# Optimization experiments

Hardware: AMD Instinct MI355X
Metric: run time of the kernel (lower is better)

## Reference

```python
import jax, jax.numpy as jnp
import numpy as np

B, NH, M, XD = 8192, 128, 4096, 1024
ALPHA_1, SIGMA_1 = 100.0, 0.02
MAX_ITER = 30  # FastBarrierProjectionNoUpper(max_iter=30)


def cayley(W):
    """Cayley orthogonalization of a (possibly rectangular) matrix (out, in)."""
    cout, cin = W.shape
    if cout < cin:
        return cayley(W.T).T
    U, V = W[:cin], W[cin:]                 # U: (cin,cin), V: (cout-cin,cin)
    I = jnp.eye(cin, dtype=W.dtype)
    A = U - U.T + V.T @ V                   # skew + Gram
    iIpA = jnp.linalg.inv(I + A)
    return jnp.concatenate([iIpA @ (I - A), -2.0 * V @ iIpA], axis=0)


def cayley_linear(x, W, b, alpha):
    Q = cayley(alpha * W / jnp.linalg.norm(W))
    return x @ Q.T + b


def project_no_upper(lower, f_tilde):
    """Projection of f_tilde onto {f : sum(f)=0, f >= lower} per row.
    f*(lam) = max(f_tilde - lam, lower); Newton on g(lam)=sum f*(lam)=0,
    iterated a fixed MAX_ITER times (matches the 30-iter barrier solver)."""
    lam0 = jnp.mean(f_tilde, axis=-1, keepdims=True)

    def step(lam, _):
        f = jnp.maximum(f_tilde - lam, lower)
        g = jnp.sum(f, axis=-1, keepdims=True)
        active = jnp.sum((f_tilde - lam > lower).astype(f.dtype), axis=-1, keepdims=True)
        dg = -jnp.maximum(active, 1.0)      # g'(lam), safeguarded
        return lam - g / dg, None

    lam, _ = jax.lax.scan(step, lam0, None, length=MAX_ITER)
    return jnp.maximum(f_tilde - lam, lower)


def setup_inputs() -> dict:
    key = jax.random.key(0)
    ks = jax.random.split(key, 8)
    h = jax.random.uniform(ks[0], (B, NH), dtype=jnp.float32)
    h = h / jnp.sum(h, axis=-1, keepdims=True)      # state lives on the simplex
    x = jax.random.normal(ks[1], (B, XD), dtype=jnp.float32)

    def mk_w(k, shape):
        return jax.random.normal(k, shape, dtype=jnp.float32) * 0.05

    W_hm = mk_w(ks[2], (M, NH))
    W_mm = mk_w(ks[3], (M, M))
    W_mh = mk_w(ks[4], (NH, M))
    W_ux = mk_w(ks[5], (M, XD))
    b_hm = jnp.zeros((M,), jnp.float32)
    b_mm = jnp.zeros((M,), jnp.float32)
    b_mh = jnp.zeros((NH,), jnp.float32)
    b_ux = jnp.zeros((M,), jnp.float32)
    # CayleyLinear alpha initialized to ||W||_F (so alpha*W/||W|| == W at init)
    a_hm = jnp.linalg.norm(W_hm)
    a_mm = jnp.linalg.norm(W_mm)
    a_mh = jnp.linalg.norm(W_mh)
    a_ux = jnp.linalg.norm(W_ux)
    return {"h": h, "x": x,
            "W_hm": W_hm, "b_hm": b_hm, "a_hm": a_hm,
            "W_mm": W_mm, "b_mm": b_mm, "a_mm": a_mm,
            "W_mh": W_mh, "b_mh": b_mh, "a_mh": a_mh,
            "W_ux": W_ux, "b_ux": b_ux, "a_ux": a_ux}


def reference(h, x, W_hm, b_hm, a_hm, W_mm, b_mm, a_mm,
              W_mh, b_mh, a_mh, W_ux, b_ux, a_ux):
    # _h_dot_raw (dropout identity in eval mode)
    z = cayley_linear(h, W_hm, b_hm, a_hm) + cayley_linear(x, W_ux, b_ux, a_ux)
    z = jax.nn.relu(z)
    z = jax.nn.relu(cayley_linear(z, W_mm, b_mm, a_mm))
    f_tilde = cayley_linear(z, W_mh, b_mh, a_mh)   # [B, NH]
    # barrier lower bound keeping h >= 0 forward-invariant
    lower = -ALPHA_1 * (jnp.exp(SIGMA_1 * h) - 1.0)
    return project_no_upper(lower, f_tilde)
```

## Files before the change

kernel.cpp:

```cpp
#include <hip/hip_runtime.h>
#include <math.h>

#define ALPHA_1 100.0f
#define SIGMA_1 0.02f

typedef unsigned short bf16_t;
typedef short  bf16x8  __attribute__((ext_vector_type(8)));
typedef float  floatx4 __attribute__((ext_vector_type(4)));

typedef __attribute__((address_space(1))) void glb_void;
typedef __attribute__((address_space(3))) void lds_void;

__device__ __forceinline__ float bf2f(bf16_t u){ return __uint_as_float(((unsigned)u)<<16); }
__device__ __forceinline__ bf16_t f2bf(float f){
  unsigned u = __float_as_uint(f);
  u += 0x7FFFu + ((u>>16)&1u);
  return (bf16_t)(u>>16);
}

__device__ __forceinline__ void split4(float4 v, ushort4& h, ushort4& l){
  h.x=f2bf(v.x); h.y=f2bf(v.y); h.z=f2bf(v.z); h.w=f2bf(v.w);
  l.x=f2bf(v.x-bf2f(h.x)); l.y=f2bf(v.y-bf2f(h.y));
  l.z=f2bf(v.z-bf2f(h.z)); l.w=f2bf(v.w-bf2f(h.w));
}

__device__ __forceinline__ float4 load4f(const float* p){ return *(const float4*)p; }
__device__ __forceinline__ float loadS(const float* p){ return *p; }
__device__ __forceinline__ float loadS(const bf16_t* p){ return bf2f(*p); }
__device__ __forceinline__ void storeS(float* p, float v){ *p = v; }
__device__ __forceinline__ void storeS(bf16_t* p, float v){ *p = f2bf(v); }

__device__ __forceinline__ void async_copy16(void* lds, const void* g){
  __builtin_amdgcn_global_load_lds((glb_void*)g, (lds_void*)lds, 16, 0, 0);
}

template<typename TC, int RELU>
__global__ __launch_bounds__(256) void mfma_nt_kernel(
    int Mm, int Nn, int Kk,
    const bf16_t* __restrict__ A, int lda,
    const bf16_t* __restrict__ B, int ldb,
    TC* __restrict__ C, int ldc,
    const float* __restrict__ bias)
{
  __shared__ bf16_t As[128*64];
  __shared__ bf16_t Bs[128*64];
  const int tid  = threadIdx.x;
  const int lane = tid & 63, wv = tid >> 6;
  const int m0 = (int)(blockIdx.y << 7), n0 = (int)(blockIdx.x << 7);
  const int wm = (wv >> 1) << 6, wn = (wv & 1) << 6;
  const int rbase = wv << 5;

  floatx4 acc[4][4] = {};

  for (int kk = 0; kk < Kk; kk += 64){
    __syncthreads();
#pragma unroll
    for (int q=0;q<4;q++){
      int row = rbase + (q<<3) + (lane>>3);
      int cg  = (lane&7) ^ (row&7);
      async_copy16(&As[(size_t)(rbase+(q<<3))<<6],
                   A + (size_t)(m0+row)*lda + kk + (cg<<3));
      async_copy16(&Bs[(size_t)(rbase+(q<<3))<<6],
                   B + (size_t)(n0+row)*ldb + kk + (cg<<3));
    }
    __syncthreads();
#pragma unroll
    for (int ks=0; ks<2; ks++){
      bf16x8 af[4], bf[4];
      int quad = lane>>4, mr = lane&15;
      int c = quad + (ks<<2);
#pragma unroll
      for (int i=0;i<4;i++){
        int rowa = wm + i*16 + mr;
        af[i] = *(const bf16x8*)&As[(rowa<<6) + ((c ^ (rowa&7))<<3)];
        int rowb = wn + i*16 + mr;
        bf[i] = *(const bf16x8*)&Bs[(rowb<<6) + ((c ^ (rowb&7))<<3)];
      }
#pragma unroll
      for (int i=0;i<4;i++)
#pragma unroll
        for (int j=0;j<4;j++)
          acc[i][j] = __builtin_amdgcn_mfma_f32_16x16x32_bf16(af[i], bf[j], acc[i][j], 0,0,0);
    }
  }
#pragma unroll
  for (int i=0;i<4;i++){
#pragma unroll
    for (int j=0;j<4;j++){
      int rbase2 = m0 + wm + i*16 + (lane>>4)*4;
      int col    = n0 + wn + j*16 + (lane&15);
      float bv = bias ? bias[col] : 0.0f;
#pragma unroll
      for (int r=0;r<4;r++){
        float v = acc[i][j][r] + bv;
        if (RELU) v = fmaxf(v, 0.0f);
        storeS(&C[(size_t)(rbase2+r)*ldc + col], v);
      }
    }
  }
}

template<typename TC>
__global__ __launch_bounds__(256) void fgemm_nt_kernel(
    int Mm, int Nn, int Kk,
    const float* __restrict__ A, int lda,
    const float* __restrict__ Bt, int ldb,
    TC* __restrict__ C, int ldc,
    float alpha, const float* __restrict__ alpha_ptr, float beta, int skipk)
{
  __shared__ bf16_t Ah[128*64], Al[128*64], Bh[128*64], Bl[128*64];
  const int tid = threadIdx.x;
  const int lane = tid & 63, wv = tid >> 6;
  int by = blockIdx.y; if (by >= skipk) by++;
  const int m0 = by << 7, n0 = blockIdx.x << 7;
  const int wm = (wv >> 1) << 6, wn = (wv & 1) << 6;
  floatx4 acc[4][4] = {};

  for (int kk = 0; kk < Kk; kk += 64){
    float4 va[8], vb[8];
#pragma unroll
    for (int i=0;i<8;i++){
      int idx = (tid<<3) + i;
      int row = idx >> 4;
      int cg  = idx & 15;
      va[i] = load4f(A  + (size_t)(m0+row)*lda + kk + (cg<<2));
      vb[i] = load4f(Bt + (size_t)(n0+row)*ldb + kk + (cg<<2));
    }
    __syncthreads();
#pragma unroll
    for (int i=0;i<8;i++){
      int idx = (tid<<3) + i;
      int row = idx >> 4, cg = idx & 15;
      int off = (row<<6) + (((cg>>1) ^ (row&7))<<3) + ((cg&1)<<2);
      ushort4 hv, lv; split4(va[i], hv, lv);
      *(ushort4*)&Ah[off] = hv; *(ushort4*)&Al[off] = lv;
      ushort4 hw, lw; split4(vb[i], hw, lw);
      *(ushort4*)&Bh[off] = hw; *(ushort4*)&Bl[off] = lw;
    }
    __syncthreads();
#pragma unroll
    for (int ks=0; ks<2; ks++){
      int quad = lane>>4, mr = lane&15;
      int c = quad + (ks<<2);
      bf16x8 ah[4], al[4], bh[4], bl[4];
#pragma unroll
      for (int i=0;i<4;i++){
        int rowa = wm + i*16 + mr; int sa = (rowa<<6) + ((c ^ (rowa&7))<<3);
        ah[i] = *(const bf16x8*)&Ah[sa]; al[i] = *(const bf16x8*)&Al[sa];
        int rowb = wn + i*16 + mr; int sb = (rowb<<6) + ((c ^ (rowb&7))<<3);
        bh[i] = *(const bf16x8*)&Bh[sb]; bl[i] = *(const bf16x8*)&Bl[sb];
      }
#pragma unroll
      for (int i=0;i<4;i++)
#pragma unroll
        for (int j=0;j<4;j++){
          acc[i][j] = __builtin_amdgcn_mfma_f32_16x16x32_bf16(ah[i], bl[j], acc[i][j], 0,0,0);
          acc[i][j] = __builtin_amdgcn_mfma_f32_16x16x32_bf16(al[i], bh[j], acc[i][j], 0,0,0);
          acc[i][j] = __builtin_amdgcn_mfma_f32_16x16x32_bf16(ah[i], bh[j], acc[i][j], 0,0,0);
        }
    }
    __syncthreads();
  }
  float am = alpha;
  if (alpha_ptr) am *= *alpha_ptr;
#pragma unroll
  for (int i=0;i<4;i++){
#pragma unroll
    for (int j=0;j<4;j++){
      int rb = m0 + wm + i*16 + (lane>>4)*4;
      int col = n0 + wn + j*16 + (lane&15);
#pragma unroll
      for (int r=0;r<4;r++){
        size_t off = (size_t)(rb+r)*ldc + col;
        float v = am * acc[i][j][r];
        if (beta != 0.0f) v = fmaf(beta, loadS(&C[off]), v);
        storeS(&C[off], v);
      }
    }
  }
}

__global__ __launch_bounds__(1024) void invert128_kernel(
    const float* __restrict__ src, int ld,
    float* __restrict__ dst, float* __restrict__ dstT)
{
  __shared__ float brow[2][8*36];
  const int t = threadIdx.x;
  const int r = t>>3, sub = t&7;
  const int lane = t & 63;
  const int cb = (sub&3)<<5;
  const bool isA = sub < 4;
  float own[32];
  if (isA){
#pragma unroll
    for (int i=0;i<32;i++) own[i] = src[(size_t)r*ld + cb + i];
  } else {
#pragma unroll
    for (int i=0;i<32;i++) own[i] = (cb+i == r) ? 1.0f : 0.0f;
  }
  for (int pb=0; pb<4; pb++){
#pragma unroll
    for (int pi=0; pi<32; pi++){
      const int p = (pb<<5) + pi;
      float f = __shfl(own[pi], (lane & 56) | pb);
      float* bw = brow[p & 1];
      if (r == p){
        float ip = 1.0f / f;
#pragma unroll
        for (int i=0;i<32;i++) own[i] *= ip;
#pragma unroll
        for (int i=0;i<8;i++){
          float4 v;
          v.x = own[(i<<2)+0]; v.y = own[(i<<2)+1];
          v.z = own[(i<<2)+2]; v.w = own[(i<<2)+3];
          *(float4*)&bw[sub*36 + (i<<2)] = v;
        }
      }
      __syncthreads();
      if (r != p){
#pragma unroll
        for (int i=0;i<8;i++){
          float4 b = *(const float4*)&bw[sub*36 + (i<<2)];
          own[(i<<2)+0] = fmaf(-f, b.x, own[(i<<2)+0]);
          own[(i<<2)+1] = fmaf(-f, b.y, own[(i<<2)+1]);
          own[(i<<2)+2] = fmaf(-f, b.z, own[(i<<2)+2]);
          own[(i<<2)+3] = fmaf(-f, b.w, own[(i<<2)+3]);
        }
      }
    }
  }
  if (!isA){
#pragma unroll
    for (int i=0;i<32;i++){
      dst [(size_t)r*128 + cb + i] = own[i];
      dstT[(size_t)(cb+i)*128 + r] = own[i];
    }
  }
}


__device__ void prep1024(
    const float* __restrict__ Mc, int n, int k, int ib,
    bf16_t* __restrict__ Gh, bf16_t* __restrict__ Gl,
    bf16_t* __restrict__ Th, bf16_t* __restrict__ Tl,
    char* smraw, int t)
{
  float* browB = (float*)smraw;
  float* Pl    = (float*)(smraw + 2304);
  float* Ast   = (float*)(smraw + 69888);
  const int r = t>>3, sub = t&7;
  const int lane = t & 63;
  const int cb = (sub&3)<<5;
  const bool isA = sub < 4;
  const float* D = Mc + ((size_t)(k<<7))*n + (k<<7);
  float own[32];
  if (isA){
#pragma unroll
    for (int q=0;q<32;q++) own[q] = D[(size_t)r*n + cb + q];
  } else {
#pragma unroll
    for (int q=0;q<32;q++) own[q] = (cb+q == r) ? 1.0f : 0.0f;
  }
  for (int pb=0; pb<4; pb++){
#pragma unroll
    for (int pi=0; pi<32; pi++){
      const int p = (pb<<5) + pi;
      float f = __shfl(own[pi], (lane & 56) | pb);
      float* bw = browB + (p & 1)*288;
      if (r == p){
        float ip = 1.0f / f;
#pragma unroll
        for (int q=0;q<32;q++) own[q] *= ip;
#pragma unroll
        for (int q=0;q<8;q++){
          float4 v;
          v.x=own[(q<<2)+0]; v.y=own[(q<<2)+1]; v.z=own[(q<<2)+2]; v.w=own[(q<<2)+3];
          *(float4*)&bw[sub*36 + (q<<2)] = v;
        }
      }
      __syncthreads();
      if (r != p){
#pragma unroll
        for (int q=0;q<8;q++){
          float4 b = *(const float4*)&bw[sub*36 + (q<<2)];
          own[(q<<2)+0] = fmaf(-f, b.x, own[(q<<2)+0]);
          own[(q<<2)+1] = fmaf(-f, b.y, own[(q<<2)+1]);
          own[(q<<2)+2] = fmaf(-f, b.z, own[(q<<2)+2]);
          own[(q<<2)+3] = fmaf(-f, b.w, own[(q<<2)+3]);
        }
      }
    }
  }
  if (!isA){
#pragma unroll
    for (int q=0;q<8;q++){
      float4 v;
      v.x=own[(q<<2)+0]; v.y=own[(q<<2)+1]; v.z=own[(q<<2)+2]; v.w=own[(q<<2)+3];
      *(float4*)&Pl[r*132 + cb + (q<<2)] = v;
      if (ib == k){
        ushort4 hv, lv; split4(v, hv, lv);
        *(ushort4*)&Gh[((size_t)k<<14) + (r<<7) + cb + (q<<2)] = hv;
        *(ushort4*)&Gl[((size_t)k<<14) + (r<<7) + cb + (q<<2)] = lv;
      }
    }
  }
  __syncthreads();
  if (ib == k) return;

  const float* Ski = Mc + ((size_t)(k<<7))*n + (ib<<7);
#pragma unroll
  for (int q=0;q<4;q++){
    int f4 = (t<<2) + q;
    int rr = f4>>5, c4 = (f4&31)<<2;
    *(float4*)&Ast[rr*132 + c4] = *(const float4*)&Ski[(size_t)rr*n + c4];
  }
  __syncthreads();
#pragma unroll
  for (int q=0;q<4;q++){
    int f4 = (t<<2) + q;
    int cc = f4>>5, r4 = (f4&31)<<2;
    float4 v;
    v.x = Ast[(r4+0)*132 + cc]; v.y = Ast[(r4+1)*132 + cc];
    v.z = Ast[(r4+2)*132 + cc]; v.w = Ast[(r4+3)*132 + cc];
    ushort4 hv, lv; split4(v, hv, lv);
    *(ushort4*)&Th[((size_t)ib<<14) + (cc<<7) + r4] = hv;
    *(ushort4*)&Tl[((size_t)ib<<14) + (cc<<7) + r4] = lv;
  }
  __syncthreads();

  const float* Sik = Mc + ((size_t)(ib<<7))*n + (k<<7);
#pragma unroll
  for (int q=0;q<4;q++){
    int f4 = (t<<2) + q;
    int rr = f4>>5, c4 = (f4&31)<<2;
    *(float4*)&Ast[rr*132 + c4] = *(const float4*)&Sik[(size_t)rr*n + c4];
  }
  __syncthreads();

  const int tx = t&31, ty = t>>5;
  const int r0 = ty<<2, c0 = tx<<2;
  float acc[4][4] = {};
  for (int kq=0; kq<128; kq++){
    float4 b = *(const float4*)&Pl[kq*132 + c0];
    float a0 = Ast[(r0+0)*132 + kq];
    float a1 = Ast[(r0+1)*132 + kq];
    float a2 = Ast[(r0+2)*132 + kq];
    float a3 = Ast[(r0+3)*132 + kq];
    acc[0][0]=fmaf(a0,b.x,acc[0][0]); acc[0][1]=fmaf(a0,b.y,acc[0][1]);
    acc[0][2]=fmaf(a0,b.z,acc[0][2]); acc[0][3]=fmaf(a0,b.w,acc[0][3]);
    acc[1][0]=fmaf(a1,b.x,acc[1][0]); acc[1][1]=fmaf(a1,b.y,acc[1][1]);
    acc[1][2]=fmaf(a1,b.z,acc[1][2]); acc[1][3]=fmaf(a1,b.w,acc[1][3]);
    acc[2][0]=fmaf(a2,b.x,acc[2][0]); acc[2][1]=fmaf(a2,b.y,acc[2][1]);
    acc[2][2]=fmaf(a2,b.z,acc[2][2]); acc[2][3]=fmaf(a2,b.w,acc[2][3]);
    acc[3][0]=fmaf(a3,b.x,acc[3][0]); acc[3][1]=fmaf(a3,b.y,acc[3][1]);
    acc[3][2]=fmaf(a3,b.z,acc[3][2]); acc[3][3]=fmaf(a3,b.w,acc[3][3]);
  }
#pragma unroll
  for (int rr=0;rr<4;rr++){
    float4 v; v.x=-acc[rr][0]; v.y=-acc[rr][1]; v.z=-acc[rr][2]; v.w=-acc[rr][3];
    ushort4 hv, lv; split4(v, hv, lv);
    *(ushort4*)&Gh[((size_t)ib<<14) + ((size_t)(r0+rr)<<7) + c0] = hv;
    *(ushort4*)&Gl[((size_t)ib<<14) + ((size_t)(r0+rr)<<7) + c0] = lv;
  }
}

__device__ void update_tile1024(
    const float* __restrict__ Min, float* __restrict__ Mout, int n, int k,
    int by, int bx,
    const bf16_t* __restrict__ Gh, const bf16_t* __restrict__ Gl,
    const bf16_t* __restrict__ Th, const bf16_t* __restrict__ Tl,
    char* sm, int tid)
{
  if (bx == k){
    const bf16_t* sh = Gh + ((size_t)by<<14);
    const bf16_t* sl = Gl + ((size_t)by<<14);
    float* dst = Mout + ((size_t)(by<<7))*n + ((size_t)k<<7);
    for (int q=tid; q<4096; q+=1024){
      int r=q>>5, c4=(q&31)<<2;
      ushort4 hv=*(const ushort4*)&sh[(r<<7)+c4];
      ushort4 lv=*(const ushort4*)&sl[(r<<7)+c4];
      float4 v; v.x=bf2f(hv.x)+bf2f(lv.x); v.y=bf2f(hv.y)+bf2f(lv.y);
                v.z=bf2f(hv.z)+bf2f(lv.z); v.w=bf2f(hv.w)+bf2f(lv.w);
      *(float4*)&dst[(size_t)r*n + c4] = v;
    }
    return;
  }
  bf16_t* Ah=(bf16_t*)sm;           bf16_t* Al=(bf16_t*)(sm+16384);
  bf16_t* Bh=(bf16_t*)(sm+32768);   bf16_t* Bl=(bf16_t*)(sm+49152);
  const int lane = tid & 63, wv = tid >> 6;
  const int wm = (wv >> 2) << 5, wn = (wv & 3) << 5;
  const bf16_t* gh = Gh + ((size_t)by<<14);
  const bf16_t* gl = Gl + ((size_t)by<<14);
  const bf16_t* th = Th + ((size_t)bx<<14);
  const bf16_t* tl = Tl + ((size_t)bx<<14);
  floatx4 acc[2][2] = {};

#pragma unroll
  for (int kk = 0; kk < 128; kk += 64){
    __syncthreads();
#pragma unroll
    for (int s=0;s<2;s++){
      int idx = tid + (s<<10);
      int row = idx >> 4, cg = idx & 15;
      int off = (row<<6) + (((cg>>1) ^ (row&7))<<3) + ((cg&1)<<2);
      *(ushort4*)&Ah[off] = *(const ushort4*)&gh[(row<<7) + kk + (cg<<2)];
      *(ushort4*)&Al[off] = *(const ushort4*)&gl[(row<<7) + kk + (cg<<2)];
      *(ushort4*)&Bh[off] = *(const ushort4*)&th[(row<<7) + kk + (cg<<2)];
      *(ushort4*)&Bl[off] = *(const ushort4*)&tl[(row<<7) + kk + (cg<<2)];
    }
    __syncthreads();
#pragma unroll
    for (int ks=0; ks<2; ks++){
      int quad = lane>>4, mr = lane&15;
      int c = quad + (ks<<2);
      bf16x8 ah[2], al[2], bh[2], bl[2];
#pragma unroll
      for (int i=0;i<2;i++){
        int rowa = wm + i*16 + mr; int sa = (rowa<<6) + ((c ^ (rowa&7))<<3);
        ah[i] = *(const bf16x8*)&Ah[sa]; al[i] = *(const bf16x8*)&Al[sa];
        int rowb = wn + i*16 + mr; int sb = (rowb<<6) + ((c ^ (rowb&7))<<3);
        bh[i] = *(const bf16x8*)&Bh[sb]; bl[i] = *(const bf16x8*)&Bl[sb];
      }
#pragma unroll
      for (int i=0;i<2;i++)
#pragma unroll
        for (int j=0;j<2;j++){
          acc[i][j] = __builtin_amdgcn_mfma_f32_16x16x32_bf16(ah[i], bl[j], acc[i][j], 0,0,0);
          acc[i][j] = __builtin_amdgcn_mfma_f32_16x16x32_bf16(al[i], bh[j], acc[i][j], 0,0,0);
          acc[i][j] = __builtin_amdgcn_mfma_f32_16x16x32_bf16(ah[i], bh[j], acc[i][j], 0,0,0);
        }
    }
  }
  const int addin = (by != k);
#pragma unroll
  for (int i=0;i<2;i++)
#pragma unroll
    for (int j=0;j<2;j++){
      int rb = (by<<7) + wm + i*16 + ((lane>>4)<<2);
      int col = (bx<<7) + wn + j*16 + (lane&15);
#pragma unroll
      for (int r4=0;r4<4;r4++){
        size_t off = (size_t)(rb+r4)*n + col;
        float v = acc[i][j][r4];
        if (addin) v += Min[off];
        Mout[off] = v;
      }
    }
}

__global__ __launch_bounds__(1024) void gj_prep0_kernel(
    const float* __restrict__ M, int n,
    bf16_t* Gh, bf16_t* Gl, bf16_t* Th, bf16_t* Tl)
{
  __shared__ char sm[137472] __attribute__((aligned(16)));
  prep1024(M, n, 0, blockIdx.x, Gh, Gl, Th, Tl, sm, threadIdx.x);
}

__global__ __launch_bounds__(1024) void gj_stepA_kernel(
    const float* __restrict__ Min, float* __restrict__ Mout, int n, int k,
    const bf16_t* __restrict__ Gh, const bf16_t* __restrict__ Gl,
    const bf16_t* __restrict__ Th, const bf16_t* __restrict__ Tl)
{
  __shared__ char sm[65536] __attribute__((aligned(16)));
  const int nb = n >> 7;
  const int bid = blockIdx.x;
  int by, bx;
  if (bid < nb){ by = bid; bx = k+1; }
  else { by = k+1; bx = bid-nb; if (bx >= k+1) bx++; }
  update_tile1024(Min, Mout, n, k, by, bx, Gh, Gl, Th, Tl, sm, threadIdx.x);
}

__global__ __launch_bounds__(1024) void gj_stepB_kernel(
    const float* __restrict__ Min, float* __restrict__ Mout, int n, int k,
    const bf16_t* __restrict__ Gh, const bf16_t* __restrict__ Gl,
    const bf16_t* __restrict__ Th, const bf16_t* __restrict__ Tl,
    bf16_t* Gnh, bf16_t* Gnl, bf16_t* Tnh, bf16_t* Tnl)
{
  __shared__ char sm[137472] __attribute__((aligned(16)));
  const int nb = n >> 7;
  const int bid = blockIdx.x, tid = threadIdx.x;
  if (bid < nb){
    prep1024(Mout, n, k+1, bid, Gnh, Gnl, Tnh, Tnl, sm, tid);
  } else {
    int q = bid - nb;
    int by = q/(nb-1), bx = q - by*(nb-1);
    if (by >= k+1) by++;
    if (bx >= k+1) bx++;
    update_tile1024(Min, Mout, n, k, by, bx, Gh, Gl, Th, Tl, sm, tid);
  }
}

__global__ __launch_bounds__(1024) void gj_stepL_kernel(
    const float* __restrict__ Min, float* __restrict__ Mout, int n, int k,
    const bf16_t* __restrict__ Gh, const bf16_t* __restrict__ Gl,
    const bf16_t* __restrict__ Th, const bf16_t* __restrict__ Tl)
{
  __shared__ char sm[65536] __attribute__((aligned(16)));
  const int nb = n >> 7;
  int by = blockIdx.x / nb, bx = blockIdx.x - by*nb;
  update_tile1024(Min, Mout, n, k, by, bx, Gh, Gl, Th, Tl, sm, threadIdx.x);
}

template<int TRANS>
__global__ __launch_bounds__(256) void gram_partial_kernel(
    const float* __restrict__ V, int ldv, int n, int Ks,
    float* __restrict__ Gp)
{
  __shared__ float Vi[16][132];
  __shared__ float Vj[16][132];
  const int cj = blockIdx.x, ci = blockIdx.y, z = blockIdx.z;
  const int tid = threadIdx.x;
  const int i0 = ci<<7, j0 = cj<<7;
  const int tx = tid&15, ty = tid>>4;
  float acc[8][8] = {};
  for (int k0 = z*Ks; k0 < (z+1)*Ks; k0 += 16){
    if (TRANS == 0){
      for (int q=tid; q<512; q+=256){
        int kr = q>>5, c4 = (q&31)<<2;
        *(float4*)&Vi[kr][c4] = *(const float4*)&V[(size_t)(k0+kr)*ldv + i0 + c4];
        *(float4*)&Vj[kr][c4] = *(const float4*)&V[(size_t)(k0+kr)*ldv + j0 + c4];
      }
    } else {
      for (int q=tid; q<512; q+=256){
        int c = q>>2, qq = (q&3)<<2;
        float4 a = *(const float4*)&V[(size_t)(i0+c)*ldv + k0 + qq];
        Vi[qq+0][c]=a.x; Vi[qq+1][c]=a.y; Vi[qq+2][c]=a.z; Vi[qq+3][c]=a.w;
        float4 b = *(const float4*)&V[(size_t)(j0+c)*ldv + k0 + qq];
        Vj[qq+0][c]=b.x; Vj[qq+1][c]=b.y; Vj[qq+2][c]=b.z; Vj[qq+3][c]=b.w;
      }
    }
    __syncthreads();
#pragma unroll
    for (int kr=0; kr<16; kr++){
      float a[8], b[8];
      *(float4*)&a[0] = *(const float4*)&Vi[kr][(ty<<3)];
      *(float4*)&a[4] = *(const float4*)&Vi[kr][(ty<<3)+4];
      *(float4*)&b[0] = *(const float4*)&Vj[kr][(tx<<3)];
      *(float4*)&b[4] = *(const float4*)&Vj[kr][(tx<<3)+4];
#pragma unroll
      for (int i=0;i<8;i++)
#pragma unroll
        for (int jj=0;jj<8;jj++) acc[i][jj] = fmaf(a[i], b[jj], acc[i][jj]);
    }
    __syncthreads();
  }
#pragma unroll
  for (int i=0;i<8;i++)
#pragma unroll
    for (int jj=0;jj<8;jj++)
      Gp[(size_t)z*n*n + (size_t)(i0+(ty<<3)+i)*n + j0+(tx<<3)+jj] = acc[i][jj];
}

__global__ void sumsq_kernel(const float* __restrict__ w, int n, float* __restrict__ acc){
  float s = 0.0f;
  for (int i = blockIdx.x*blockDim.x + threadIdx.x; i < n; i += gridDim.x*blockDim.x){
    float v = w[i]; s = fmaf(v, v, s);
  }
#pragma unroll
  for (int o=32;o;o>>=1) s += __shfl_xor(s, o);
  if ((threadIdx.x & 63) == 0) atomicAdd(acc, s);
}

__global__ void scales_kernel(float* scal, const float* a0, const float* a1,
                              const float* a2, const float* a3){
  if (threadIdx.x==0 && blockIdx.x==0){
    float s;
    s = a0[0]/sqrtf(scal[0]); scal[4]=s; scal[8]=s*s;
    s = a1[0]/sqrtf(scal[1]); scal[5]=s; scal[9]=s*s;
    s = a2[0]/sqrtf(scal[2]); scal[6]=s; scal[10]=s*s;
    s = a3[0]/sqrtf(scal[3]); scal[7]=s; scal[11]=s*s;
  }
}

__global__ void build_mm_kernel(const float* __restrict__ W, const float* __restrict__ scal,
                                float* __restrict__ Mo){
  int j = (blockIdx.x<<4) + (threadIdx.x&15);
  int i = (blockIdx.y<<4) + (threadIdx.x>>4);
  float s = scal[5];
  float a = s*(W[((size_t)i<<12)+j] - W[((size_t)j<<12)+i]);
  Mo[((size_t)i<<12)+j] = ((i==j)?1.0f:0.0f) + a;
}

__global__ void build_rect_kernel(const float* __restrict__ W, int ldw, int transw, int n,
      const float* __restrict__ Gp, int S,
      const float* __restrict__ scal, int sidx, int sidx2,
      float* __restrict__ Mo){
  int j = (blockIdx.x<<4)+(threadIdx.x&15);
  int i = (blockIdx.y<<4)+(threadIdx.x>>4);
  float s = scal[sidx], s2 = scal[sidx2];
  float wij = transw ? W[(size_t)j*ldw+i] : W[(size_t)i*ldw+j];
  float wji = transw ? W[(size_t)i*ldw+j] : W[(size_t)j*ldw+i];
  float g = 0.0f;
  for (int ss=0; ss<S; ss++) g += Gp[(size_t)ss*n*n + (size_t)i*n + j];
  Mo[(size_t)i*n + j] = ((i==j)?1.0f:0.0f) + s*(wij - wji) + s2*g;
}

template<typename TD>
__global__ void qtop_kernel(const float* __restrict__ X, int n,
                            TD* __restrict__ dst, int ldd){
  int j = blockIdx.x*blockDim.x + threadIdx.x;
  int i = blockIdx.y;
  if (j<n) storeS(&dst[(size_t)i*ldd+j],
                  2.0f*X[(size_t)i*n+j] - ((i==j)?1.0f:0.0f));
}

__global__ void transposeF_kernel(const float* __restrict__ src, int ls,
                                  float* __restrict__ dst, int ld){
  __shared__ float t[32][33];
  int c0 = blockIdx.x<<5, r0 = blockIdx.y<<5;
  int tx = threadIdx.x & 31, ty = threadIdx.x >> 5;
#pragma unroll
  for (int i=0;i<4;i++) t[ty+i*8][tx] = src[(size_t)(r0+ty+i*8)*ls + c0+tx];
  __syncthreads();
#pragma unroll
  for (int i=0;i<4;i++) dst[(size_t)(c0+ty+i*8)*ld + r0+tx] = t[tx][ty+i*8];
}

__global__ void pack_A_kernel(const float* __restrict__ h, const float* __restrict__ x,
                              bf16_t* __restrict__ Ap){
  int c = blockIdx.x*blockDim.x + threadIdx.x;
  int m = blockIdx.y;
  if (c >= 2176) return;
  float v;
  if (c < 128)       v = h[(size_t)m*128 + c];
  else if (c < 1152) v = x[(size_t)m*1024 + (c-128)];
  else {
    float xv = x[(size_t)m*1024 + (c-1152)];
    v = xv - bf2f(f2bf(xv));
  }
  Ap[(size_t)m*2176 + c] = f2bf(v);
}

__global__ void dup_kernel(bf16_t* __restrict__ Bp){
  int c = blockIdx.x*blockDim.x + threadIdx.x;
  int r = blockIdx.y;
  Bp[(size_t)r*2176 + 1152 + c] = Bp[(size_t)r*2176 + 128 + c];
}

__global__ void addvec_kernel(const float* __restrict__ a, const float* __restrict__ b,
                              float* __restrict__ c, int n){
  int i = blockIdx.x*blockDim.x + threadIdx.x;
  if (i<n) c[i] = a[i] + b[i];
}

__global__ __launch_bounds__(256) void project_kernel(
    const float* __restrict__ ft, const float* __restrict__ h, float* __restrict__ out){
  int row  = (blockIdx.x<<2) + (threadIdx.x>>6);
  int lane = threadIdx.x & 63;
  const float* fr = ft + ((size_t)row<<7);
  const float* hr = h  + ((size_t)row<<7);
  float f0 = fr[lane], f1 = fr[lane+64];
  float l0 = -ALPHA_1*(expf(SIGMA_1*hr[lane])   - 1.0f);
  float l1 = -ALPHA_1*(expf(SIGMA_1*hr[lane+64])- 1.0f);
  float s = f0 + f1;
#pragma unroll
  for (int o=32;o;o>>=1) s += __shfl_xor(s, o);
  float lam = s * (1.0f/128.0f);
  for (int it=0; it<30; it++){
    float a0 = f0 - lam, a1 = f1 - lam;
    float g = fmaxf(a0,l0) + fmaxf(a1,l1);
    float c = (a0>l0 ? 1.0f:0.0f) + (a1>l1 ? 1.0f:0.0f);
#pragma unroll
    for (int o=32;o;o>>=1){ g += __shfl_xor(g,o); c += __shfl_xor(c,o); }
    lam += g / fmaxf(c, 1.0f);
  }
  out[((size_t)row<<7)+lane]    = fmaxf(f0-lam, l0);
  out[((size_t)row<<7)+lane+64] = fmaxf(f1-lam, l1);
}

template<typename TC, int RELU>
static inline void mfma_nt(hipStream_t st, int Mm, int Nn, int Kk,
    const bf16_t* A, int lda, const bf16_t* B, int ldb, TC* C, int ldc,
    const float* bias){
  dim3 grid(Nn>>7, Mm>>7);
  mfma_nt_kernel<TC,RELU><<<grid, 256, 0, st>>>(Mm,Nn,Kk,A,lda,B,ldb,C,ldc,bias);
}

template<typename TC>
static inline void fgemm(hipStream_t st, int Mm, int Nn, int Kk,
    const float* A, int lda, const float* Bt, int ldb, TC* C, int ldc,
    float alpha, const float* aptr, float beta){
  dim3 grid(Nn>>7, Mm>>7);
  fgemm_nt_kernel<TC><<<grid, 256, 0, st>>>(Mm,Nn,Kk,A,lda,Bt,ldb,C,ldc,
                                            alpha,aptr,beta, 1<<30);
}

static void gj_inverse4(hipStream_t st, float* M, float* Mtmp, int n,
    bf16_t* Gh, bf16_t* Gl, bf16_t* Th, bf16_t* Tl){
  const int nb = n >> 7;
  const size_t gstep = (size_t)nb << 14;
  gj_prep0_kernel<<<nb, 1024, 0, st>>>(M, n, Gh, Gl, Th, Tl);
  for (int k=0; k<nb; k++){
    const float* Min = (k&1) ? Mtmp : M;
    float* Mout      = (k&1) ? M : Mtmp;
    const size_t pc = (size_t)(k&1)*gstep, pn = (size_t)((k&1)^1)*gstep;
    if (k < nb-1){
      gj_stepA_kernel<<<2*nb-1, 1024, 0, st>>>(Min, Mout, n, k,
          Gh+pc, Gl+pc, Th+pc, Tl+pc);
      gj_stepB_kernel<<<nb + (nb-1)*(nb-1), 1024, 0, st>>>(Min, Mout, n, k,
          Gh+pc, Gl+pc, Th+pc, Tl+pc,
          Gh+pn, Gl+pn, Th+pn, Tl+pn);
    } else {
      gj_stepL_kernel<<<nb*nb, 1024, 0, st>>>(Min, Mout, n, k,
          Gh+pc, Gl+pc, Th+pc, Tl+pc);
    }
  }
}

extern "C" void kernel_launch(void* const* d_in, const int* in_sizes, int n_in,
                              void* d_out, int out_size, void* d_ws, size_t ws_size,
                              hipStream_t stream){
  (void)in_sizes; (void)n_in; (void)out_size; (void)ws_size;
  const float* h    = (const float*)d_in[0];
  const float* x    = (const float*)d_in[1];
  const float* Whm  = (const float*)d_in[2];
  const float* bhm  = (const float*)d_in[3];
  const float* ahm  = (const float*)d_in[4];
  const float* Wmm  = (const float*)d_in[5];
  const float* bmm  = (const float*)d_in[6];
  const float* amm  = (const float*)d_in[7];
  const float* Wmh  = (const float*)d_in[8];
  const float* bmh  = (const float*)d_in[9];
  const float* amh  = (const float*)d_in[10];
  const float* Wux  = (const float*)d_in[11];
  const float* bux  = (const float*)d_in[12];
  const float* auxs = (const float*)d_in[13];
  float* out = (float*)d_out;

  char* wp = (char*)d_ws;
  auto alloc = [&](size_t bytes)->void*{
    void* p = (void*)wp; wp += (bytes + 255) & ~(size_t)255; return p; };
  float*  scal   = (float*)alloc(4096);
  float*  Mhm    = (float*)alloc((size_t)128*128*4);
  float*  Mmh    = (float*)alloc((size_t)128*128*4);
  float*  P128   = (float*)alloc((size_t)128*128*4);
  float*  PT128  = (float*)alloc((size_t)128*128*4);
  bf16_t* GhB    = (bf16_t*)alloc((size_t)2*32*16384*2);
  bf16_t* GlB    = (bf16_t*)alloc((size_t)2*32*16384*2);
  bf16_t* ThB    = (bf16_t*)alloc((size_t)2*32*16384*2);
  bf16_t* TlB    = (bf16_t*)alloc((size_t)2*32*16384*2);
  bf16_t* Qmh_b  = (bf16_t*)alloc((size_t)128*4096*2);
  float*  bsum   = (float*)alloc((size_t)4096*4);
  bf16_t* Bp     = (bf16_t*)alloc((size_t)4096*2176*2);
  float*  R1     = (float*)alloc((size_t)4096*4096*4);
  float*  R2     = (float*)alloc((size_t)4096*4096*4);
  bf16_t* Qmmb   = (bf16_t*)alloc((size_t)4096*4096*2);
  float*  gram23 = R1;
  float*  WmhTv  = R1 + (size_t)1024*1024;
  float*  Mmm  = R1;
  bf16_t* Ap   = (bf16_t*)R1;
  bf16_t* z2   = (bf16_t*)R1;
  float*  Mux  = R2 + (size_t)1024*1024;
  float*  XuxT = R2 + (size_t)5*1024*1024;
  float*  Gp1  = R2 + (size_t)6*1024*1024;
  bf16_t* z    = (bf16_t*)R2;
  float*  ftl  = R2;

  hipMemsetAsync(scal, 0, 16*sizeof(float), stream);
  sumsq_kernel<<<512,256,0,stream>>>(Whm, 4096*128,  scal+0);
  sumsq_kernel<<<512,256,0,stream>>>(Wmm, 4096*4096, scal+1);
  sumsq_kernel<<<512,256,0,stream>>>(Wmh, 128*4096,  scal+2);
  sumsq_kernel<<<512,256,0,stream>>>(Wux, 4096*1024, scal+3);
  scales_kernel<<<1,1,0,stream>>>(scal, ahm, amm, amh, auxs);

  gram_partial_kernel<0><<<dim3(8,8,4),256,0,stream>>>(
      Wux + (size_t)1024*1024, 1024, 1024, 768, Gp1);
  build_rect_kernel<<<dim3(64,64),256,0,stream>>>(Wux,1024,0,1024, Gp1,4, scal,7,11, Mux);
  gj_inverse4(stream, Mux, R1, 1024, GhB, GlB, ThB, TlB);
  transposeF_kernel<<<dim3(32,32),256,0,stream>>>(Mux, 1024, XuxT, 1024);
  qtop_kernel<bf16_t><<<dim3(4,1024),256,0,stream>>>(Mux, 1024, Bp+128, 2176);
  fgemm<bf16_t>(stream, 3072,1024,1024, Wux+(size_t)1024*1024,1024, XuxT,1024,
                Bp+(size_t)1024*2176+128, 2176, -2.0f,&scal[7], 0.0f);

  gram_partial_kernel<0><<<dim3(1,1,31),256,0,stream>>>(
      Whm + (size_t)128*128, 128, 128, 128, gram23);
  build_rect_kernel<<<dim3(8,8),256,0,stream>>>(Whm,128,0,128, gram23,31, scal,4,8, Mhm);
  invert128_kernel<<<1,1024,0,stream>>>(Mhm,128,P128,PT128);
  qtop_kernel<bf16_t><<<dim3(1,128),256,0,stream>>>(P128, 128, Bp, 2176);
  fgemm<bf16_t>(stream, 3968,128,128, Whm+128*128,128, PT128,128,
                Bp+(size_t)128*2176, 2176, -2.0f,&scal[4], 0.0f);

  gram_partial_kernel<1><<<dim3(1,1,31),256,0,stream>>>(
      Wmh + 128, 4096, 128, 128, gram23);
  build_rect_kernel<<<dim3(8,8),256,0,stream>>>(Wmh,4096,1,128, gram23,31, scal,6,10, Mmh);
  invert128_kernel<<<1,1024,0,stream>>>(Mmh,128,P128,PT128);
  qtop_kernel<bf16_t><<<dim3(1,128),256,0,stream>>>(PT128, 128, Qmh_b, 4096);
  transposeF_kernel<<<dim3(124,4),256,0,stream>>>(Wmh+128, 4096, WmhTv, 128);
  fgemm<bf16_t>(stream, 128,3968,128, PT128,128, WmhTv,128,
                Qmh_b+128, 4096, -2.0f,&scal[6], 0.0f);

  build_mm_kernel<<<dim3(256,256),256,0,stream>>>(Wmm, scal, Mmm);
  gj_inverse4(stream, Mmm, R2, 4096, GhB, GlB, ThB, TlB);
  qtop_kernel<bf16_t><<<dim3(16,4096),256,0,stream>>>(Mmm, 4096, Qmmb, 4096);

  pack_A_kernel<<<dim3(9,8192),256,0,stream>>>(h, x, Ap);
  dup_kernel<<<dim3(4,4096),256,0,stream>>>(Bp);
  addvec_kernel<<<16,256,0,stream>>>(bhm, bux, bsum, 4096);

  mfma_nt<bf16_t,1>(stream, 8192,4096,2176, Ap,2176, Bp,2176, z,4096, bsum);
  mfma_nt<bf16_t,1>(stream, 8192,4096,4096, z,4096, Qmmb,4096, z2,4096, bmm);
  mfma_nt<float,0>(stream, 8192, 128,4096, z2,4096, Qmh_b,4096, ftl,128, bmh);

  project_kernel<<<2048,256,0,stream>>>(ftl, h, out);
}
```

Measured before the change: 5.696 ms.

## Fuse Gauss-Jordan pivot-panel prep into a single per-step kernel

```diff
diff --git a/kernel.cpp b/kernel.cpp
--- a/kernel.cpp
+++ b/kernel.cpp
@@ -238,6 +238,89 @@
   }
 }
 
+
+__device__ void tile_to_lds(
+    const float* __restrict__ Min, int n, int k, int r, int c,
+    const bf16_t* __restrict__ Gh, const bf16_t* __restrict__ Gl,
+    const bf16_t* __restrict__ Th, const bf16_t* __restrict__ Tl,
+    float* __restrict__ Dst, char* __restrict__ stage, int tid)
+{
+  if (c == k){
+    const bf16_t* sh = Gh + ((size_t)r<<14);
+    const bf16_t* sl = Gl + ((size_t)r<<14);
+    for (int q=tid; q<4096; q+=1024){
+      int rr=q>>5, c4=(q&31)<<2;
+      ushort4 hv=*(const ushort4*)&sh[(rr<<7)+c4];
+      ushort4 lv=*(const ushort4*)&sl[(rr<<7)+c4];
+      Dst[rr*132+c4+0]=bf2f(hv.x)+bf2f(lv.x);
+      Dst[rr*132+c4+1]=bf2f(hv.y)+bf2f(lv.y);
+      Dst[rr*132+c4+2]=bf2f(hv.z)+bf2f(lv.z);
+      Dst[rr*132+c4+3]=bf2f(hv.w)+bf2f(lv.w);
+    }
+    __syncthreads();
+    return;
+  }
+  bf16_t* Ah=(bf16_t*)stage;           bf16_t* Al=(bf16_t*)(stage+16384);
+  bf16_t* Bh=(bf16_t*)(stage+32768);   bf16_t* Bl=(bf16_t*)(stage+49152);
+  const int lane = tid & 63, wv = tid >> 6;
+  const int wm = (wv >> 2) << 5, wn = (wv & 3) << 5;
+  const bf16_t* gh = Gh + ((size_t)r<<14);
+  const bf16_t* gl = Gl + ((size_t)r<<14);
+  const bf16_t* th = Th + ((size_t)c<<14);
+  const bf16_t* tl = Tl + ((size_t)c<<14);
+  floatx4 acc[2][2] = {};
+#pragma unroll
+  for (int kk = 0; kk < 128; kk += 64){
+    __syncthreads();
+#pragma unroll
+    for (int s=0;s<2;s++){
+      int idx = tid + (s<<10);
+      int row = idx >> 4, cg = idx & 15;
+      int off = (row<<6) + (((cg>>1) ^ (row&7))<<3) + ((cg&1)<<2);
+      *(ushort4*)&Ah[off] = *(const ushort4*)&gh[(row<<7) + kk + (cg<<2)];
+      *(ushort4*)&Al[off] = *(const ushort4*)&gl[(row<<7) + kk + (cg<<2)];
+      *(ushort4*)&Bh[off] = *(const ushort4*)&th[(row<<7) + kk + (cg<<2)];
+      *(ushort4*)&Bl[off] = *(const ushort4*)&tl[(row<<7) + kk + (cg<<2)];
+    }
+    __syncthreads();
+#pragma unroll
+    for (int ks=0; ks<2; ks++){
+      int quad = lane>>4, mr = lane&15;
+      int cc = quad + (ks<<2);
+      bf16x8 ah[2], al[2], bh[2], bl[2];
+#pragma unroll
+      for (int i=0;i<2;i++){
+        int rowa = wm + i*16 + mr; int sa = (rowa<<6) + ((cc ^ (rowa&7))<<3);
+        ah[i] = *(const bf16x8*)&Ah[sa]; al[i] = *(const bf16x8*)&Al[sa];
+        int rowb = wn + i*16 + mr; int sb = (rowb<<6) + ((cc ^ (rowb&7))<<3);
+        bh[i] = *(const bf16x8*)&Bh[sb]; bl[i] = *(const bf16x8*)&Bl[sb];
+      }
+#pragma unroll
+      for (int i=0;i<2;i++)
+#pragma unroll
+        for (int j=0;j<2;j++){
+          acc[i][j] = __builtin_amdgcn_mfma_f32_16x16x32_bf16(ah[i], bl[j], acc[i][j], 0,0,0);
+          acc[i][j] = __builtin_amdgcn_mfma_f32_16x16x32_bf16(al[i], bh[j], acc[i][j], 0,0,0);
+          acc[i][j] = __builtin_amdgcn_mfma_f32_16x16x32_bf16(ah[i], bh[j], acc[i][j], 0,0,0);
+        }
+    }
+  }
+  const int addin = (r != k);
+#pragma unroll
+  for (int i=0;i<2;i++)
+#pragma unroll
+    for (int j=0;j<2;j++){
+      int rb = wm + i*16 + ((lane>>4)<<2);
+      int col = wn + j*16 + (lane&15);
+#pragma unroll
+      for (int r4=0;r4<4;r4++){
+        float v = acc[i][j][r4];
+        if (addin) v += Min[(size_t)((r<<7)+rb+r4)*n + (c<<7) + col];
+        Dst[(rb+r4)*132 + col] = v;
+      }
+    }
+  __syncthreads();
+}
 
 __device__ void prep1024(
     const float* __restrict__ Mc, int n, int k, int ib,
@@ -364,6 +447,133 @@
   }
 }
 
+__device__ void prep_fused(
+    const float* __restrict__ Min, int n, int k, int ib,
+    const bf16_t* __restrict__ Gh, const bf16_t* __restrict__ Gl,
+    const bf16_t* __restrict__ Th, const bf16_t* __restrict__ Tl,
+    bf16_t* __restrict__ Gnh, bf16_t* __restrict__ Gnl,
+    bf16_t* __restrict__ Tnh, bf16_t* __restrict__ Tnl,
+    char* smraw, int t)
+{
+  const int kp = k+1;
+  float* browB = (float*)smraw;
+  float* Pl    = (float*)(smraw + 2304);
+  float* Ast   = (float*)(smraw + 69888);
+  char*  stage = (char*)(smraw + 2304);
+
+  tile_to_lds(Min, n, k, kp, kp, Gh, Gl, Th, Tl, Ast, stage, t);
+
+  const int r = t>>3, sub = t&7;
+  const int lane = t & 63;
+  const int cb = (sub&3)<<5;
+  const bool isA = sub < 4;
+  float own[32];
+  if (isA){
+#pragma unroll
+    for (int q=0;q<8;q++)
+      *(float4*)&own[q<<2] = *(const float4*)&Ast[r*132 + cb + (q<<2)];
+  } else {
+#pragma unroll
+    for (int q=0;q<32;q++) own[q] = (cb+q == r) ? 1.0f : 0.0f;
+  }
+  __syncthreads();
+  for (int pb=0; pb<4; pb++){
+#pragma unroll
+    for (int pi=0; pi<32; pi++){
+      const int p = (pb<<5) + pi;
+      float f = __shfl(own[pi], (lane & 56) | pb);
+      float* bw = browB + (p & 1)*288;
+      if (r == p){
+        float ip = 1.0f / f;
+#pragma unroll
+        for (int q=0;q<32;q++) own[q] *= ip;
+#pragma unroll
+        for (int q=0;q<8;q++){
+          float4 v;
+          v.x=own[(q<<2)+0]; v.y=own[(q<<2)+1]; v.z=own[(q<<2)+2]; v.w=own[(q<<2)+3];
+          *(float4*)&bw[sub*36 + (q<<2)] = v;
+        }
+      }
+      __syncthreads();
+      if (r != p){
+#pragma unroll
+        for (int q=0;q<8;q++){
+          float4 b = *(const float4*)&bw[sub*36 + (q<<2)];
+          own[(q<<2)+0] = fmaf(-f, b.x, own[(q<<2)+0]);
+          own[(q<<2)+1] = fmaf(-f, b.y, own[(q<<2)+1]);
+          own[(q<<2)+2] = fmaf(-f, b.z, own[(q<<2)+2]);
+          own[(q<<2)+3] = fmaf(-f, b.w, own[(q<<2)+3]);
+        }
+      }
+    }
+  }
+  if (ib == kp){
+    if (!isA){
+#pragma unroll
+      for (int q=0;q<8;q++){
+        float4 v;
+        v.x=own[(q<<2)+0]; v.y=own[(q<<2)+1]; v.z=own[(q<<2)+2]; v.w=own[(q<<2)+3];
+        ushort4 hv, lv; split4(v, hv, lv);
+        *(ushort4*)&Gnh[((size_t)kp<<14) + (r<<7) + cb + (q<<2)] = hv;
+        *(ushort4*)&Gnl[((size_t)kp<<14) + (r<<7) + cb + (q<<2)] = lv;
+      }
+    }
+    return;
+  }
+
+  tile_to_lds(Min, n, k, kp, ib, Gh, Gl, Th, Tl, Ast, stage, t);
+#pragma unroll
+  for (int q=0;q<4;q++){
+    int f4 = (t<<2) + q;
+    int cc = f4>>5, r4 = (f4&31)<<2;
+    float4 v;
+    v.x = Ast[(r4+0)*132 + cc]; v.y = Ast[(r4+1)*132 + cc];
+    v.z = Ast[(r4+2)*132 + cc]; v.w = Ast[(r4+3)*132 + cc];
+    ushort4 hv, lv; split4(v, hv, lv);
+    *(ushort4*)&Tnh[((size_t)ib<<14) + (cc<<7) + r4] = hv;
+    *(ushort4*)&Tnl[((size_t)ib<<14) + (cc<<7) + r4] = lv;
+  }
+  __syncthreads();
+
+  tile_to_lds(Min, n, k, ib, kp, Gh, Gl, Th, Tl, Ast, stage, t);
+
+  if (!isA){
+#pragma unroll
+    for (int q=0;q<8;q++){
+      float4 v;
+      v.x=own[(q<<2)+0]; v.y=own[(q<<2)+1]; v.z=own[(q<<2)+2]; v.w=own[(q<<2)+3];
+      *(float4*)&Pl[r*132 + cb + (q<<2)] = v;
+    }
+  }
+  __syncthreads();
+
+  const int tx = t&31, ty = t>>5;
+  const int r0 = ty<<2, c0 = tx<<2;
+  float acc[4][4] = {};
+  for (int kq=0; kq<128; kq++){
+    float4 b = *(const float4*)&Pl[kq*132 + c0];
+    float a0 = Ast[(r0+0)*132 + kq];
+    float a1 = Ast[(r0+1)*132 + kq];
+    float a2 = Ast[(r0+2)*132 + kq];
+    float a3 = Ast[(r0+3)*132 + kq];
+    acc[0][0]=fmaf(a0,b.x,acc[0][0]); acc[0][1]=fmaf(a0,b.y,acc[0][1]);
+    acc[0][2]=fmaf(a0,b.z,acc[0][2]); acc[0][3]=fmaf(a0,b.w,acc[0][3]);
+    acc[1][0]=fmaf(a1,b.x,acc[1][0]); acc[1][1]=fmaf(a1,b.y,acc[1][1]);
+    acc[1][2]=fmaf(a1,b.z,acc[1][2]); acc[1][3]=fmaf(a1,b.w,acc[1][3]);
+    acc[2][0]=fmaf(a2,b.x,acc[2][0]); acc[2][1]=fmaf(a2,b.y,acc[2][1]);
+    acc[2][2]=fmaf(a2,b.z,acc[2][2]); acc[2][3]=fmaf(a2,b.w,acc[2][3]);
+    acc[3][0]=fmaf(a3,b.x,acc[3][0]); acc[3][1]=fmaf(a3,b.y,acc[3][1]);
+    acc[3][2]=fmaf(a3,b.z,acc[3][2]); acc[3][3]=fmaf(a3,b.w,acc[3][3]);
+  }
+#pragma unroll
+  for (int rr=0;rr<4;rr++){
+    float4 v; v.x=-acc[rr][0]; v.y=-acc[rr][1]; v.z=-acc[rr][2]; v.w=-acc[rr][3];
+    ushort4 hv, lv; split4(v, hv, lv);
+    *(ushort4*)&Gnh[((size_t)ib<<14) + ((size_t)(r0+rr)<<7) + c0] = hv;
+    *(ushort4*)&Gnl[((size_t)ib<<14) + ((size_t)(r0+rr)<<7) + c0] = lv;
+  }
+}
+
 __device__ void update_tile1024(
     const float* __restrict__ Min, float* __restrict__ Mout, int n, int k,
     int by, int bx,
@@ -456,21 +666,7 @@
   prep1024(M, n, 0, blockIdx.x, Gh, Gl, Th, Tl, sm, threadIdx.x);
 }
 
-__global__ __launch_bounds__(1024) void gj_stepA_kernel(
-    const float* __restrict__ Min, float* __restrict__ Mout, int n, int k,
-    const bf16_t* __restrict__ Gh, const bf16_t* __restrict__ Gl,
-    const bf16_t* __restrict__ Th, const bf16_t* __restrict__ Tl)
-{
-  __shared__ char sm[65536] __attribute__((aligned(16)));
-  const int nb = n >> 7;
-  const int bid = blockIdx.x;
-  int by, bx;
-  if (bid < nb){ by = bid; bx = k+1; }
-  else { by = k+1; bx = bid-nb; if (bx >= k+1) bx++; }
-  update_tile1024(Min, Mout, n, k, by, bx, Gh, Gl, Th, Tl, sm, threadIdx.x);
-}
-
-__global__ __launch_bounds__(1024) void gj_stepB_kernel(
+__global__ __launch_bounds__(1024) void gj_stepF_kernel(
     const float* __restrict__ Min, float* __restrict__ Mout, int n, int k,
     const bf16_t* __restrict__ Gh, const bf16_t* __restrict__ Gl,
     const bf16_t* __restrict__ Th, const bf16_t* __restrict__ Tl,
@@ -480,12 +676,10 @@
   const int nb = n >> 7;
   const int bid = blockIdx.x, tid = threadIdx.x;
   if (bid < nb){
-    prep1024(Mout, n, k+1, bid, Gnh, Gnl, Tnh, Tnl, sm, tid);
+    prep_fused(Min, n, k, bid, Gh, Gl, Th, Tl, Gnh, Gnl, Tnh, Tnl, sm, tid);
   } else {
     int q = bid - nb;
-    int by = q/(nb-1), bx = q - by*(nb-1);
-    if (by >= k+1) by++;
-    if (bx >= k+1) bx++;
+    int by = q / nb, bx = q - by*nb;
     update_tile1024(Min, Mout, n, k, by, bx, Gh, Gl, Th, Tl, sm, tid);
   }
 }
@@ -685,7 +879,7 @@
                                             alpha,aptr,beta, 1<<30);
 }
 
-static void gj_inverse4(hipStream_t st, float* M, float* Mtmp, int n,
+static void gj_inverse5(hipStream_t st, float* M, float* Mtmp, int n,
     bf16_t* Gh, bf16_t* Gl, bf16_t* Th, bf16_t* Tl){
   const int nb = n >> 7;
   const size_t gstep = (size_t)nb << 14;
@@ -695,9 +889,7 @@
     float* Mout      = (k&1) ? M : Mtmp;
     const size_t pc = (size_t)(k&1)*gstep, pn = (size_t)((k&1)^1)*gstep;
     if (k < nb-1){
-      gj_stepA_kernel<<<2*nb-1, 1024, 0, st>>>(Min, Mout, n, k,
-          Gh+pc, Gl+pc, Th+pc, Tl+pc);
-      gj_stepB_kernel<<<nb + (nb-1)*(nb-1), 1024, 0, st>>>(Min, Mout, n, k,
+      gj_stepF_kernel<<<nb + nb*nb, 1024, 0, st>>>(Min, Mout, n, k,
           Gh+pc, Gl+pc, Th+pc, Tl+pc,
           Gh+pn, Gl+pn, Th+pn, Tl+pn);
     } else {
@@ -766,7 +958,7 @@
   gram_partial_kernel<0><<<dim3(8,8,4),256,0,stream>>>(
       Wux + (size_t)1024*1024, 1024, 1024, 768, Gp1);
   build_rect_kernel<<<dim3(64,64),256,0,stream>>>(Wux,1024,0,1024, Gp1,4, scal,7,11, Mux);
-  gj_inverse4(stream, Mux, R1, 1024, GhB, GlB, ThB, TlB);
+  gj_inverse5(stream, Mux, R1, 1024, GhB, GlB, ThB, TlB);
   transposeF_kernel<<<dim3(32,32),256,0,stream>>>(Mux, 1024, XuxT, 1024);
   qtop_kernel<bf16_t><<<dim3(4,1024),256,0,stream>>>(Mux, 1024, Bp+128, 2176);
   fgemm<bf16_t>(stream, 3072,1024,1024, Wux+(size_t)1024*1024,1024, XuxT,1024,
@@ -790,7 +982,7 @@
                 Qmh_b+128, 4096, -2.0f,&scal[6], 0.0f);
 
   build_mm_kernel<<<dim3(256,256),256,0,stream>>>(Wmm, scal, Mmm);
-  gj_inverse4(stream, Mmm, R2, 4096, GhB, GlB, ThB, TlB);
+  gj_inverse5(stream, Mmm, R2, 4096, GhB, GlB, ThB, TlB);
   qtop_kernel<bf16_t><<<dim3(16,4096),256,0,stream>>>(Mmm, 4096, Qmmb, 4096);
 
   pack_A_kernel<<<dim3(9,8192),256,0,stream>>>(h, x, Ap);
```

Measured after the change: 5.112 ms (median of 2 runs). 1.11x faster.
